# Optimization experiments

Measured on AMD Instinct MI355X. Metric: run time of the kernel, lower is better.

## Reference

```python
import jax, jax.numpy as jnp
import numpy as np

B, S, HID = 2, 2048, 2048
N_HEADS, N_KV, HEAD_DIM = 8, 1, 256
ROPE_THETA = 10000.0
NEG = -1e9


def setup_inputs() -> dict:
    key = jax.random.key(0)
    ks = jax.random.split(key, 6)
    hidden_states = jax.random.normal(ks[0], (B, S, HID), dtype=jnp.float32)
    position_ids = jnp.broadcast_to(jnp.arange(S, dtype=jnp.int32)[None, :], (B, S))
    causal = jnp.tril(jnp.ones((S, S), dtype=bool))
    attention_mask = jnp.where(causal, 0.0, NEG).astype(jnp.float32)[None, None]
    attention_mask = jnp.broadcast_to(attention_mask, (B, 1, S, S))
    sc = 0.02
    Wq = jax.random.normal(ks[1], (N_HEADS * HEAD_DIM, HID), dtype=jnp.float32) * sc
    Wk = jax.random.normal(ks[2], (N_KV * HEAD_DIM, HID), dtype=jnp.float32) * sc
    Wv = jax.random.normal(ks[3], (N_KV * HEAD_DIM, HID), dtype=jnp.float32) * sc
    Wo = jax.random.normal(ks[4], (HID, N_HEADS * HEAD_DIM), dtype=jnp.float32) * sc
    return {"hidden_states": hidden_states, "position_ids": position_ids,
            "attention_mask": attention_mask, "Wq": Wq, "Wk": Wk, "Wv": Wv, "Wo": Wo}


def _rotate_half(x):
    x1, x2 = jnp.split(x, 2, axis=-1)
    return jnp.concatenate((-x2, x1), axis=-1)


def _rope_cos_sin(position_ids, head_dim, dtype):
    inv_freq = 1.0 / (ROPE_THETA ** (jnp.arange(0, head_dim, 2, dtype=jnp.float32) / head_dim))
    freqs = position_ids.astype(jnp.float32)[:, :, None] * inv_freq[None, None, :]  # [B,S,D/2]
    emb = jnp.concatenate((freqs, freqs), axis=-1)  # [B,S,D]
    return jnp.cos(emb).astype(dtype), jnp.sin(emb).astype(dtype)


def reference(hidden_states, position_ids, attention_mask, Wq, Wk, Wv, Wo):
    b, s, _ = hidden_states.shape
    d = HEAD_DIM
    rep = N_HEADS // N_KV
    q = (hidden_states @ Wq.T).reshape(b, s, N_HEADS, d).transpose(0, 2, 1, 3)  # [B,H,S,D]
    k = (hidden_states @ Wk.T).reshape(b, s, N_KV, d).transpose(0, 2, 1, 3)    # [B,KV,S,D]
    v = (hidden_states @ Wv.T).reshape(b, s, N_KV, d).transpose(0, 2, 1, 3)
    cos, sin = _rope_cos_sin(position_ids, d, hidden_states.dtype)
    cos, sin = cos[:, None], sin[:, None]  # broadcast over heads
    q = q * cos + _rotate_half(q) * sin
    k = k * cos + _rotate_half(k) * sin
    # GQA: group queries per kv head, no materialized repeat
    qg = q.reshape(b, N_KV, rep, s, d)
    scores = jnp.einsum('bgrqd,bgkd->bgrqk', qg, k) / jnp.sqrt(jnp.float32(d)).astype(q.dtype)
    scores = scores.reshape(b, N_HEADS, s, s) + attention_mask
    probs = jax.nn.softmax(scores.astype(jnp.float32), axis=-1).astype(q.dtype)
    out = jnp.einsum('bgrqk,bgkd->bgrqd', probs.reshape(b, N_KV, rep, s, s), v)
    out = out.reshape(b, N_HEADS, s, d).transpose(0, 2, 1, 3).reshape(b, s, N_HEADS * d)
    return out @ Wo.T
```

## Files before the change

### kernel.cpp

```cpp
#include <hip/hip_runtime.h>
#include <hip/hip_bf16.h>

typedef __bf16 bf16x8 __attribute__((ext_vector_type(8)));
typedef float  f32x4  __attribute__((ext_vector_type(4)));

#define BATCH 2
#define SEQ   2048
#define HID   2048
#define NH    8
#define DH    256
#define LQ    2560
#define ROWS  (BATCH*SEQ)
#define KVB   32

__device__ __forceinline__ void gld16(const void* g, void* l) {
    __builtin_amdgcn_global_load_lds(
        (__attribute__((address_space(1))) void*)(g),
        (__attribute__((address_space(3))) void*)(l), 16, 0, 0);
}

__device__ __forceinline__ unsigned pack2bf(float a, float b) {
    union { __bf16 h[2]; unsigned u; } x;
    x.h[0] = (__bf16)a; x.h[1] = (__bf16)b;
    return x.u;
}

__global__ void cvt_f32_bf16(const float* __restrict__ src, __bf16* __restrict__ dst, int n4) {
    int i = blockIdx.x * blockDim.x + threadIdx.x;
    if (i < n4) {
        float4 v = ((const float4*)src)[i];
        __bf16 o[4];
        o[0] = (__bf16)v.x; o[1] = (__bf16)v.y; o[2] = (__bf16)v.z; o[3] = (__bf16)v.w;
        ((uint2*)dst)[i] = *(uint2*)o;
    }
}

template<typename CT>
__global__ __launch_bounds__(256)
void gemm_bt(const __bf16* __restrict__ A, const __bf16* __restrict__ B,
             CT* __restrict__ C, int M, int N, int K) {
    __shared__ __bf16 sA[128 * 32];
    __shared__ __bf16 sB[128 * 32];
    const int tid  = threadIdx.x;
    const int lane = tid & 63;
    const int wid  = tid >> 6;
    const int row0 = blockIdx.y * 128;
    const int col0 = blockIdx.x * 128;
    const int wr = (wid >> 1) * 64;
    const int wc = (wid & 1) * 64;

    const int sr0 = tid >> 2, sc0 = (tid & 3) * 8;
    const __bf16* Ag0 = A + (size_t)(row0 + sr0) * K + sc0;
    const __bf16* Ag1 = Ag0 + (size_t)64 * K;
    const __bf16* Bg0 = B + (size_t)(col0 + sr0) * K + sc0;
    const __bf16* Bg1 = Bg0 + (size_t)64 * K;
    __bf16* lA0 = &sA[wid * 512];
    __bf16* lA1 = &sA[2048 + wid * 512];
    __bf16* lB0 = &sB[wid * 512];
    __bf16* lB1 = &sB[2048 + wid * 512];

    f32x4 acc[4][4];
#pragma unroll
    for (int m = 0; m < 4; ++m)
#pragma unroll
        for (int n = 0; n < 4; ++n) acc[m][n] = (f32x4)0.f;

    for (int k0 = 0; k0 < K; k0 += 32) {
        gld16(Ag0 + k0, lA0);
        gld16(Ag1 + k0, lA1);
        gld16(Bg0 + k0, lB0);
        gld16(Bg1 + k0, lB1);
        __syncthreads();
        bf16x8 af[4], bfr[4];
#pragma unroll
        for (int m = 0; m < 4; ++m)
            af[m] = *(const bf16x8*)&sA[(wr + m * 16 + (lane & 15)) * 32 + (lane >> 4) * 8];
#pragma unroll
        for (int n = 0; n < 4; ++n)
            bfr[n] = *(const bf16x8*)&sB[(wc + n * 16 + (lane & 15)) * 32 + (lane >> 4) * 8];
#pragma unroll
        for (int m = 0; m < 4; ++m)
#pragma unroll
            for (int n = 0; n < 4; ++n)
                acc[m][n] = __builtin_amdgcn_mfma_f32_16x16x32_bf16(af[m], bfr[n], acc[m][n], 0, 0, 0);
        __syncthreads();
    }
#pragma unroll
    for (int m = 0; m < 4; ++m)
#pragma unroll
        for (int n = 0; n < 4; ++n)
#pragma unroll
            for (int r = 0; r < 4; ++r) {
                int row = row0 + wr + m * 16 + (lane >> 4) * 4 + r;
                int col = col0 + wc + n * 16 + (lane & 15);
                C[(size_t)row * N + col] = (CT)acc[m][n][r];
            }
}

__global__ void rope_kernel(__bf16* __restrict__ QKV, const int* __restrict__ pid) {
    const int row = blockIdx.x;
    const int h   = blockIdx.y;
    const int j   = threadIdx.x;
    const float pos = (float)pid[row];
    const float freq = exp2f((float)j * (-13.287712379549449f / 128.0f));
    const float ang = pos * freq;
    float sn, cs;
    sincosf(ang, &sn, &cs);
    const float sc = (h < 8) ? 0.0625f : 1.0f;
    __bf16* p = QKV + (size_t)row * LQ + h * 256 + j;
    float x1 = (float)p[0], x2 = (float)p[128];
    p[0]   = (__bf16)((x1 * cs - x2 * sn) * sc);
    p[128] = (__bf16)((x2 * cs + x1 * sn) * sc);
}

__global__ __launch_bounds__(256)
void transpose_v(const __bf16* __restrict__ QKV, __bf16* __restrict__ Vt) {
    __shared__ __bf16 t[32][33];
    const int b  = blockIdx.z;
    const int s0 = blockIdx.x * 32;
    const int d0 = blockIdx.y * 32;
    const int c  = threadIdx.x & 31;
    const int r8 = threadIdx.x >> 5;
#pragma unroll
    for (int i = 0; i < 4; ++i) {
        int row = r8 + i * 8;
        t[row][c] = QKV[(size_t)(b * SEQ + s0 + row) * LQ + 2304 + d0 + c];
    }
    __syncthreads();
#pragma unroll
    for (int i = 0; i < 4; ++i) {
        int row = r8 + i * 8;
        Vt[((size_t)b * 256 + d0 + row) * SEQ + s0 + c] = t[c][row];
    }
}

__global__ __launch_bounds__(512, 2)
void attn_fwd5(const __bf16* __restrict__ QKV, const __bf16* __restrict__ Vt,
               __bf16* __restrict__ A0, __bf16* __restrict__ A1,
               float2* __restrict__ ML) {
    __shared__ __bf16 Kt[2][KVB * 256];
    __shared__ __bf16 Vs[2][256 * KVB];
    __shared__ char   Pl[8][16 * 80];

    const int tid  = threadIdx.x;
    const int lane = tid & 63;
    const int wid  = tid >> 6;
    const int lc   = lane & 15;
    const int l4   = lane >> 4;

    const int bid = blockIdx.x;
    const int b   = bid >> 7;
    const int pg  = bid & 63;
    const int kvh = (bid >> 6) & 1;
    const int h   = wid;

    const char* QKVb = (const char*)(QKV + (size_t)(b * SEQ) * LQ);
    const char* Kg   = QKVb + 2048 * 2;
    const char* Vg   = (const char*)(Vt + (size_t)b * DH * SEQ);

    const int kr0   = wid * 4 + (lane >> 5);
    const int kcolb = (lane & 31) * 16;
    const int vd0   = wid * 32 + (lane >> 2);
    const int vcol0 = (lane & 3) * 16;
    const int vrsw  = ((lc >> 1) & 3) << 4;
    char* Pw = &Pl[wid][0];

#define STAGE(B_, KV0) do {                                                         \
    _Pragma("unroll")                                                               \
    for (int i_ = 0; i_ < 2; ++i_) {                                                \
        int r_ = kr0 + i_ * 2;                                                      \
        gld16(Kg + (size_t)((KV0) + r_) * (LQ * 2) + (kcolb ^ ((r_ & 7) << 4)),     \
              (char*)&Kt[B_][0] + (wid * 2 + i_) * 1024);                           \
    }                                                                               \
    _Pragma("unroll")                                                               \
    for (int i_ = 0; i_ < 2; ++i_) {                                                \
        int d_ = vd0 + i_ * 16;                                                     \
        gld16(Vg + (size_t)d_ * (SEQ * 2) + (KV0) * 2 + (vcol0 ^ (((d_ >> 1) & 3) << 4)), \
              (char*)&Vs[B_][0] + (wid * 2 + i_) * 1024);                           \
    }                                                                               \
} while (0)

    for (int seg = 0; seg < 2; ++seg) {
        const int c    = seg ? (127 - pg) : pg;
        const int ntc  = (c >> 1) + 1;
        const int t0   = kvh ? (ntc >> 1) : 0;
        const int t1   = kvh ? ntc : (ntc >> 1);
        const int q0   = c * 16;
        const int qrow = q0 + lc;

        const char* Qp = QKVb + (size_t)(q0 + lc) * (LQ * 2) + h * 512 + l4 * 16;
        bf16x8 qf[8];
#pragma unroll
        for (int kc = 0; kc < 8; ++kc) qf[kc] = *(const bf16x8*)(Qp + kc * 64);

        f32x4 oacc[16];
#pragma unroll
        for (int i = 0; i < 16; ++i) oacc[i] = (f32x4)0.f;
        float mrow = -1e30f, lrow = 0.f;

        __syncthreads();
        if (t0 < t1) {
            STAGE(0, t0 * KVB);
            int buf = 0;
            for (int t = t0; t < t1; ++t) {
                __syncthreads();
                const int kv0 = t * KVB;
                if (t + 1 < t1) STAGE(buf ^ 1, kv0 + KVB);

                f32x4 sacc[2];
                sacc[0] = (f32x4)0.f; sacc[1] = (f32x4)0.f;
                const char* Kl = (const char*)&Kt[buf][0];
                __builtin_amdgcn_s_setprio(1);
#pragma unroll
                for (int kc = 0; kc < 8; ++kc) {
#pragma unroll
                    for (int ct = 0; ct < 2; ++ct) {
                        const int rr = ct * 16 + lc;
                        bf16x8 kf = *(const bf16x8*)(Kl + rr * 512 +
                                                     (((kc << 6) | (l4 << 4)) ^ ((rr & 7) << 4)));
                        sacc[ct] = __builtin_amdgcn_mfma_f32_16x16x32_bf16(kf, qf[kc], sacc[ct], 0, 0, 0);
                    }
                }
                __builtin_amdgcn_s_setprio(0);

                const bool lastt = (t == ntc - 1);
                float tm = -1e30f;
#pragma unroll
                for (int ct = 0; ct < 2; ++ct)
#pragma unroll
                    for (int r = 0; r < 4; ++r) {
                        float s = sacc[ct][r];
                        if (lastt) {
                            int kv = kv0 + ct * 16 + l4 * 4 + r;
                            if (kv > qrow) s = -1e30f;
                        }
                        sacc[ct][r] = s;
                        tm = fmaxf(tm, s);
                    }
                tm = fmaxf(tm, __shfl_xor(tm, 16, 64));
                tm = fmaxf(tm, __shfl_xor(tm, 32, 64));
                if (!__all(tm <= mrow + 8.f)) {
                    const float mnew  = fmaxf(mrow, tm);
                    const float alpha = __expf(mrow - mnew);
                    mrow = mnew;
                    lrow *= alpha;
#pragma unroll
                    for (int dt = 0; dt < 16; ++dt) {
                        oacc[dt][0] *= alpha; oacc[dt][1] *= alpha;
                        oacc[dt][2] *= alpha; oacc[dt][3] *= alpha;
                    }
                }
                float p0[4], p1[4], ps = 0.f;
#pragma unroll
                for (int r = 0; r < 4; ++r) { p0[r] = __expf(sacc[0][r] - mrow); ps += p0[r]; }
#pragma unroll
                for (int r = 0; r < 4; ++r) { p1[r] = __expf(sacc[1][r] - mrow); ps += p1[r]; }
                ps += __shfl_xor(ps, 16, 64);
                ps += __shfl_xor(ps, 32, 64);
                lrow += ps;

                *(uint2*)(Pw + lc * 80 + l4 * 8) =
                    make_uint2(pack2bf(p0[0], p0[1]), pack2bf(p0[2], p0[3]));
                *(uint2*)(Pw + lc * 80 + 32 + l4 * 8) =
                    make_uint2(pack2bf(p1[0], p1[1]), pack2bf(p1[2], p1[3]));
                asm volatile("s_waitcnt lgkmcnt(0)" ::: "memory");
                __builtin_amdgcn_sched_barrier(0);
                bf16x8 pb = *(const bf16x8*)(Pw + lc * 80 + l4 * 16);

                const char* Vl = (const char*)&Vs[buf][0];
                __builtin_amdgcn_s_setprio(1);
#pragma unroll
                for (int dt = 0; dt < 16; ++dt) {
                    bf16x8 vf = *(const bf16x8*)(Vl + (dt * 16 + lc) * 64 + ((l4 << 4) ^ vrsw));
                    oacc[dt] = __builtin_amdgcn_mfma_f32_16x16x32_bf16(vf, pb, oacc[dt], 0, 0, 0);
                }
                __builtin_amdgcn_s_setprio(0);
                buf ^= 1;
            }
        }

        __bf16* dst = kvh ? A1 : A0;
        char* Op = (char*)dst + ((size_t)(b * SEQ + q0 + lc) * HID + h * 256 + l4 * 4) * 2;
#pragma unroll
        for (int dt = 0; dt < 16; ++dt) {
            __bf16 o4[4];
            o4[0] = (__bf16)oacc[dt][0];
            o4[1] = (__bf16)oacc[dt][1];
            o4[2] = (__bf16)oacc[dt][2];
            o4[3] = (__bf16)oacc[dt][3];
            *(uint2*)(Op + dt * 32) = *(uint2*)o4;
        }
        if (l4 == 0)
            ML[(size_t)kvh * ROWS * NH + (size_t)(b * SEQ + q0 + lc) * NH + h] =
                make_float2(mrow, lrow);
    }
#undef STAGE
}

__global__ __launch_bounds__(256)
void merge_attn(__bf16* __restrict__ A0, const __bf16* __restrict__ A1,
                const float2* __restrict__ ML) {
    const int idx = blockIdx.x * 256 + threadIdx.x;
    const int r = idx >> 8;
    const int g = idx & 255;
    const int h = g >> 5;
    const float2 ml0 = ML[(size_t)r * NH + h];
    const float2 ml1 = ML[(size_t)ROWS * NH + (size_t)r * NH + h];
    const float M  = fmaxf(ml0.x, ml1.x);
    float w0 = __expf(ml0.x - M), w1 = __expf(ml1.x - M);
    const float inv = 1.0f / (ml0.y * w0 + ml1.y * w1);
    w0 *= inv; w1 *= inv;
    const size_t off = (size_t)r * HID + (size_t)g * 8;
    bf16x8 a0 = *(const bf16x8*)(A0 + off);
    bf16x8 a1 = *(const bf16x8*)(A1 + off);
    bf16x8 o;
#pragma unroll
    for (int j = 0; j < 8; ++j)
        o[j] = (__bf16)((float)a0[j] * w0 + (float)a1[j] * w1);
    *(bf16x8*)(A0 + off) = o;
}

extern "C" void kernel_launch(void* const* d_in, const int* in_sizes, int n_in,
                              void* d_out, int out_size, void* d_ws, size_t ws_size,
                              hipStream_t stream) {
    const float* hs  = (const float*)d_in[0];
    const int*   pid = (const int*)d_in[1];
    const float* Wq  = (const float*)d_in[3];
    const float* Wk  = (const float*)d_in[4];
    const float* Wv  = (const float*)d_in[5];
    const float* Wo  = (const float*)d_in[6];
    float* out = (float*)d_out;

    char* ws = (char*)d_ws;
    __bf16* Xb    = (__bf16*)ws;                      ws += (size_t)ROWS * HID * 2;
    __bf16* Wqkv  = (__bf16*)ws;                      ws += (size_t)LQ * HID * 2;
    __bf16* Wob   = (__bf16*)ws;                      ws += (size_t)HID * HID * 2;
    __bf16* QKV   = (__bf16*)ws;                      ws += (size_t)ROWS * LQ * 2;
    __bf16* Vt    = (__bf16*)ws;                      ws += (size_t)BATCH * DH * SEQ * 2;
    __bf16* Apart = (__bf16*)ws;                      ws += (size_t)ROWS * HID * 2;
    float2* ML    = (float2*)ws;                      ws += (size_t)2 * ROWS * NH * sizeof(float2);
    __bf16* Oat   = Xb;

    cvt_f32_bf16<<<(ROWS * HID / 4 + 255) / 256, 256, 0, stream>>>(hs, Xb, ROWS * HID / 4);
    cvt_f32_bf16<<<(HID * HID / 4 + 255) / 256, 256, 0, stream>>>(Wq, Wqkv, HID * HID / 4);
    cvt_f32_bf16<<<(DH * HID / 4 + 255) / 256, 256, 0, stream>>>(Wk, Wqkv + (size_t)2048 * HID, DH * HID / 4);
    cvt_f32_bf16<<<(DH * HID / 4 + 255) / 256, 256, 0, stream>>>(Wv, Wqkv + (size_t)2304 * HID, DH * HID / 4);
    cvt_f32_bf16<<<(HID * HID / 4 + 255) / 256, 256, 0, stream>>>(Wo, Wob, HID * HID / 4);

    gemm_bt<__bf16><<<dim3(LQ / 128, ROWS / 128), 256, 0, stream>>>(Xb, Wqkv, QKV, ROWS, LQ, HID);

    rope_kernel<<<dim3(ROWS, 9), 128, 0, stream>>>(QKV, pid);

    transpose_v<<<dim3(SEQ / 32, DH / 32, BATCH), 256, 0, stream>>>(QKV, Vt);

    attn_fwd5<<<dim3(256), 512, 0, stream>>>(QKV, Vt, Oat, Apart, ML);

    merge_attn<<<dim3(ROWS * HID / 8 / 256), 256, 0, stream>>>(Oat, Apart, ML);

    gemm_bt<float><<<dim3(HID / 128, ROWS / 128), 256, 0, stream>>>(Oat, Wob, out, ROWS, HID, HID);
}
```

Baseline: 360.6 us.

## Replace GEMM with 256x256-tile, 4-stage pipelined, swizzled LDS kernel

```diff
diff --git a/kernel.cpp b/kernel.cpp
--- a/kernel.cpp
+++ b/kernel.cpp
@@ -36,64 +36,101 @@
 }
 
 template<typename CT>
-__global__ __launch_bounds__(256)
-void gemm_bt(const __bf16* __restrict__ A, const __bf16* __restrict__ B,
-             CT* __restrict__ C, int M, int N, int K) {
-    __shared__ __bf16 sA[128 * 32];
-    __shared__ __bf16 sB[128 * 32];
+__global__ __launch_bounds__(512, 2)
+void gemm256(const __bf16* __restrict__ A, const __bf16* __restrict__ B,
+             CT* __restrict__ C, int M, int N, int K, int gn) {
+    __shared__ __align__(16) char lds[4][32768];
     const int tid  = threadIdx.x;
     const int lane = tid & 63;
     const int wid  = tid >> 6;
-    const int row0 = blockIdx.y * 128;
-    const int col0 = blockIdx.x * 128;
-    const int wr = (wid >> 1) * 64;
-    const int wc = (wid & 1) * 64;
-
-    const int sr0 = tid >> 2, sc0 = (tid & 3) * 8;
-    const __bf16* Ag0 = A + (size_t)(row0 + sr0) * K + sc0;
-    const __bf16* Ag1 = Ag0 + (size_t)64 * K;
-    const __bf16* Bg0 = B + (size_t)(col0 + sr0) * K + sc0;
-    const __bf16* Bg1 = Bg0 + (size_t)64 * K;
-    __bf16* lA0 = &sA[wid * 512];
-    __bf16* lA1 = &sA[2048 + wid * 512];
-    __bf16* lB0 = &sB[wid * 512];
-    __bf16* lB1 = &sB[2048 + wid * 512];
-
-    f32x4 acc[4][4];
-#pragma unroll
-    for (int m = 0; m < 4; ++m)
+    const int lc = lane & 15, l4 = lane >> 4;
+
+    const int cpx = gridDim.x >> 3;
+    const int wg  = (blockIdx.x & 7) * cpx + (blockIdx.x >> 3);
+    const int row0 = (wg / gn) << 8;
+    const int col0 = (wg % gn) << 8;
+
+    int rr[2], jj[2];
+#pragma unroll
+    for (int i = 0; i < 2; ++i) {
+        int D = i * 512 + tid, rp = D >> 3, u = (D & 7) ^ (rp & 7);
+        rr[i] = (rp << 1) | (u >> 2);
+        jj[i] = u & 3;
+    }
+    const char* As0 = (const char*)A + ((size_t)(row0 + rr[0]) * K + jj[0] * 8) * 2;
+    const char* As1 = (const char*)A + ((size_t)(row0 + rr[1]) * K + jj[1] * 8) * 2;
+    const char* Bs0 = (const char*)B + ((size_t)(col0 + rr[0]) * K + jj[0] * 8) * 2;
+    const char* Bs1 = (const char*)B + ((size_t)(col0 + rr[1]) * K + jj[1] * 8) * 2;
+    const int dst16 = tid * 16;
+
+#define GSTAGE(bf_, tt_) do {                                   \
+    size_t ko_ = (size_t)(tt_) * 64;                            \
+    gld16(As0 + ko_, &lds[bf_][0]     + dst16);                 \
+    gld16(As1 + ko_, &lds[bf_][8192]  + dst16);                 \
+    gld16(Bs0 + ko_, &lds[bf_][16384] + dst16);                 \
+    gld16(Bs1 + ko_, &lds[bf_][24576] + dst16);                 \
+} while (0)
+
+    const int wr = (wid >> 2) << 7;
+    const int wc = (wid & 3) << 6;
+
+    f32x4 acc[8][4];
+#pragma unroll
+    for (int m = 0; m < 8; ++m)
 #pragma unroll
         for (int n = 0; n < 4; ++n) acc[m][n] = (f32x4)0.f;
 
-    for (int k0 = 0; k0 < K; k0 += 32) {
-        gld16(Ag0 + k0, lA0);
-        gld16(Ag1 + k0, lA1);
-        gld16(Bg0 + k0, lB0);
-        gld16(Bg1 + k0, lB1);
-        __syncthreads();
-        bf16x8 af[4], bfr[4];
-#pragma unroll
-        for (int m = 0; m < 4; ++m)
-            af[m] = *(const bf16x8*)&sA[(wr + m * 16 + (lane & 15)) * 32 + (lane >> 4) * 8];
+    const int nt = K >> 5;
+    GSTAGE(0, 0); GSTAGE(1, 1); GSTAGE(2, 2);
+    asm volatile("s_waitcnt vmcnt(8)" ::: "memory");
+    __builtin_amdgcn_s_barrier();
+    __builtin_amdgcn_sched_barrier(0);
+
+    for (int t = 0; t < nt; ++t) {
+        const char* Ab = &lds[t & 3][0];
+        const char* Bb = &lds[t & 3][16384];
+        if (t + 3 < nt) GSTAGE((t + 3) & 3, t + 3);
+
+        bf16x8 af[8], bv[4];
+#pragma unroll
+        for (int m = 0; m < 8; ++m) {
+            int r = wr + m * 16 + lc;
+            af[m] = *(const bf16x8*)(Ab + (r >> 1) * 128 +
+                      (((((r & 1) << 2) + l4) ^ ((r >> 1) & 7)) << 4));
+        }
+#pragma unroll
+        for (int n = 0; n < 4; ++n) {
+            int r = wc + n * 16 + lc;
+            bv[n] = *(const bf16x8*)(Bb + (r >> 1) * 128 +
+                      (((((r & 1) << 2) + l4) ^ ((r >> 1) & 7)) << 4));
+        }
+        __builtin_amdgcn_s_setprio(1);
+#pragma unroll
+        for (int m = 0; m < 8; ++m)
+#pragma unroll
+            for (int n = 0; n < 4; ++n)
+                acc[m][n] = __builtin_amdgcn_mfma_f32_16x16x32_bf16(af[m], bv[n], acc[m][n], 0, 0, 0);
+        __builtin_amdgcn_s_setprio(0);
+
+        if (t + 3 < nt)      asm volatile("s_waitcnt vmcnt(8)" ::: "memory");
+        else if (t + 2 < nt) asm volatile("s_waitcnt vmcnt(4)" ::: "memory");
+        else if (t + 1 < nt) asm volatile("s_waitcnt vmcnt(0)" ::: "memory");
+        if (t + 1 < nt) {
+            __builtin_amdgcn_s_barrier();
+            __builtin_amdgcn_sched_barrier(0);
+        }
+    }
+#undef GSTAGE
+
+#pragma unroll
+    for (int m = 0; m < 8; ++m)
 #pragma unroll
         for (int n = 0; n < 4; ++n)
-            bfr[n] = *(const bf16x8*)&sB[(wc + n * 16 + (lane & 15)) * 32 + (lane >> 4) * 8];
-#pragma unroll
-        for (int m = 0; m < 4; ++m)
-#pragma unroll
-            for (int n = 0; n < 4; ++n)
-                acc[m][n] = __builtin_amdgcn_mfma_f32_16x16x32_bf16(af[m], bfr[n], acc[m][n], 0, 0, 0);
-        __syncthreads();
-    }
-#pragma unroll
-    for (int m = 0; m < 4; ++m)
-#pragma unroll
-        for (int n = 0; n < 4; ++n)
-#pragma unroll
-            for (int r = 0; r < 4; ++r) {
-                int row = row0 + wr + m * 16 + (lane >> 4) * 4 + r;
-                int col = col0 + wc + n * 16 + (lane & 15);
-                C[(size_t)row * N + col] = (CT)acc[m][n][r];
+#pragma unroll
+            for (int r4 = 0; r4 < 4; ++r4) {
+                int row = row0 + wr + m * 16 + l4 * 4 + r4;
+                int col = col0 + wc + n * 16 + lc;
+                C[(size_t)row * N + col] = (CT)acc[m][n][r4];
             }
 }
 
@@ -347,7 +384,7 @@
     cvt_f32_bf16<<<(DH * HID / 4 + 255) / 256, 256, 0, stream>>>(Wv, Wqkv + (size_t)2304 * HID, DH * HID / 4);
     cvt_f32_bf16<<<(HID * HID / 4 + 255) / 256, 256, 0, stream>>>(Wo, Wob, HID * HID / 4);
 
-    gemm_bt<__bf16><<<dim3(LQ / 128, ROWS / 128), 256, 0, stream>>>(Xb, Wqkv, QKV, ROWS, LQ, HID);
+    gemm256<__bf16><<<dim3(160), 512, 0, stream>>>(Xb, Wqkv, QKV, ROWS, LQ, HID, 10);
 
     rope_kernel<<<dim3(ROWS, 9), 128, 0, stream>>>(QKV, pid);
 
@@ -357,5 +394,5 @@
 
     merge_attn<<<dim3(ROWS * HID / 8 / 256), 256, 0, stream>>>(Oat, Apart, ML);
 
-    gemm_bt<float><<<dim3(HID / 128, ROWS / 128), 256, 0, stream>>>(Oat, Wob, out, ROWS, HID, HID);
-}
+    gemm256<float><<<dim3(128), 512, 0, stream>>>(Oat, Wob, out, ROWS, HID, HID, 8);
+}
```

After: 351.2 us. 2.6% less time.
